# Kernel optimization log

Measured on AMD Instinct MI355X. Metric: run time of the kernel, lower is better.

Reference implementation:

```python
import jax, jax.numpy as jnp
import numpy as np

B, S, E, H = 4, 2048, 2048, 16
D = E // H  # head_dim = 128
MAX_LEN = 2048


def _make_freqs():
    # standard RoPE frequencies: theta = 10000^{-2i/D}
    inv_freq = 1.0 / (10000.0 ** (np.arange(0, D, 2, dtype=np.float32) / D))  # [D/2]
    t = np.arange(MAX_LEN, dtype=np.float32)
    ang = np.outer(t, inv_freq)  # [max_len, D/2]
    cos = ang.reshape(1, MAX_LEN, 1, D // 2)
    return jnp.asarray(np.cos(cos)), jnp.asarray(np.sin(cos))


def setup_inputs() -> dict:
    key = jax.random.key(0)
    ks = jax.random.split(key, 10)
    sc = 1.0 / np.sqrt(E)
    freqs_cos, freqs_sin = _make_freqs()
    return {
        "x": jax.random.normal(ks[0], (B, S, E), dtype=jnp.float32),
        "freqs_cos": freqs_cos,
        "freqs_sin": freqs_sin,
        "wq": jax.random.normal(ks[1], (E, E), dtype=jnp.float32) * sc,
        "bq": jax.random.normal(ks[2], (E,), dtype=jnp.float32) * 0.01,
        "wk": jax.random.normal(ks[3], (E, E), dtype=jnp.float32) * sc,
        "bk": jax.random.normal(ks[4], (E,), dtype=jnp.float32) * 0.01,
        "wv": jax.random.normal(ks[5], (E, E), dtype=jnp.float32) * sc,
        "bv": jax.random.normal(ks[6], (E,), dtype=jnp.float32) * 0.01,
        "wo": jax.random.normal(ks[7], (E, E), dtype=jnp.float32) * sc,
        "bo": jax.random.normal(ks[8], (E,), dtype=jnp.float32) * 0.01,
    }


def _rope(t, cos, sin):
    # t: [B, S, H, D]; complex multiply on interleaved (even, odd) pairs
    tr = t.reshape(*t.shape[:-1], -1, 2)  # [B,S,H,D/2,2]
    xr, xi = tr[..., 0], tr[..., 1]
    rr = xr * cos - xi * sin
    ri = xr * sin + xi * cos
    return jnp.stack([rr, ri], axis=-1).reshape(t.shape)


def reference(x, freqs_cos, freqs_sin, wq, bq, wk, bk, wv, bv, wo, bo):
    b, s, _ = x.shape
    q = (x @ wq.T + bq).reshape(b, s, H, D)
    k = (x @ wk.T + bk).reshape(b, s, H, D)
    v = (x @ wv.T + bv).reshape(b, s, H, D)
    cos, sin = freqs_cos[:, :s], freqs_sin[:, :s]
    q = _rope(q, cos, sin)
    k = _rope(k, cos, sin)
    # FAITHFUL to source: q,k,v stay [B,S,H,D], so matmul contracts over D
    # producing per-position head-head scores [B,S,H,H] (no transpose to BHSD).
    qk = jnp.einsum("bshd,bsgd->bshg", q, k) / jnp.sqrt(jnp.float32(D))
    att = jax.nn.softmax(qk, axis=-1)
    att_out = jnp.einsum("bshg,bsgd->bshd", att, v)  # [B,S,H,D]
    # torch: transpose(1,2).contiguous().view(B,S,-1) -> h-major flatten
    att_out = jnp.transpose(att_out, (0, 2, 1, 3)).reshape(b, s, -1)
    return att_out @ wo.T + bo
```

## Files before the change

kernel.cpp:

```cpp
#include <hip/hip_runtime.h>
#include <stdint.h>

typedef unsigned short u16t;
typedef __attribute__((ext_vector_type(8))) short frag8;
typedef __attribute__((ext_vector_type(4))) float facc4;

#define S_LEN 2048
#define E_DIM 2048

__device__ __forceinline__ u16t f2bf(float f) {
    union { float f; uint32_t u; } c; c.f = f;
    return (u16t)((c.u + 0x7fffu + ((c.u >> 16) & 1u)) >> 16);
}

__global__ __launch_bounds__(256) void cvt_kernel(const float* __restrict__ src,
                                                  u16t* __restrict__ dst, int n4) {
    int i = blockIdx.x * 256 + threadIdx.x;
    if (i >= n4) return;
    float4 v = ((const float4*)src)[i];
    ushort4 o;
    o.x = f2bf(v.x); o.y = f2bf(v.y); o.z = f2bf(v.z); o.w = f2bf(v.w);
    ((ushort4*)dst)[i] = o;
}

__device__ __forceinline__ void gldl16(const u16t* g, u16t* l) {
    __builtin_amdgcn_global_load_lds(
        (__attribute__((address_space(1))) void*)(g),
        (__attribute__((address_space(3))) void*)(l), 16, 0, 0);
}

__device__ __forceinline__ void gemm_core(const u16t* __restrict__ A,
                                          const u16t* __restrict__ Bw,
                                          u16t* As0, u16t* As1,
                                          u16t* Bs0, u16t* Bs1,
                                          facc4 acc[4][8]) {
    const int t    = threadIdx.x;
    const int lane = t & 63;
    const int wid  = t >> 6;
    const int m16  = lane & 15;
    const int quad = lane >> 4;
    const int sw   = (m16 >> 1) & 3;
    const int wm   = (wid & 1) * 64;
    const int wn   = (wid >> 1) * 128;
    const size_t bm0 = (size_t)blockIdx.y * 128;
    const size_t bn0 = (size_t)blockIdx.x * 256;

#pragma unroll
    for (int i = 0; i < 4; ++i)
#pragma unroll
        for (int j = 0; j < 8; ++j) acc[i][j] = facc4{0.f, 0.f, 0.f, 0.f};

    const u16t* Ab = A + bm0 * E_DIM;
    const u16t* Bb = Bw + bn0 * E_DIM;

    const int l8 = lane * 8;
    const int rA0 = ((wid * 1024 + l8) >> 5);
    const int rA1 = rA0 + 16;
    const int rB0 = ((wid * 2048 + l8) >> 5);
    const int rB1 = rB0 + 16, rB2 = rB0 + 32, rB3 = rB0 + 48;
    const int c3 = lane & 3;
    const size_t gA0 = (size_t)rA0 * E_DIM + ((c3 ^ ((rA0 >> 1) & 3)) * 8);
    const size_t gA1 = (size_t)rA1 * E_DIM + ((c3 ^ ((rA1 >> 1) & 3)) * 8);
    const size_t gB0 = (size_t)rB0 * E_DIM + ((c3 ^ ((rB0 >> 1) & 3)) * 8);
    const size_t gB1 = (size_t)rB1 * E_DIM + ((c3 ^ ((rB1 >> 1) & 3)) * 8);
    const size_t gB2 = (size_t)rB2 * E_DIM + ((c3 ^ ((rB2 >> 1) & 3)) * 8);
    const size_t gB3 = (size_t)rB3 * E_DIM + ((c3 ^ ((rB3 >> 1) & 3)) * 8);
    u16t* lA0 = As0 + wid * 1024;
    u16t* lA1 = As1 + wid * 1024;
    u16t* lB0 = Bs0 + wid * 2048;
    u16t* lB1 = Bs1 + wid * 2048;

    for (int k0 = 0; k0 < E_DIM; k0 += 64) {
        __syncthreads();
        gldl16(Ab + gA0 + k0,      lA0);
        gldl16(Ab + gA1 + k0,      lA0 + 512);
        gldl16(Ab + gA0 + k0 + 32, lA1);
        gldl16(Ab + gA1 + k0 + 32, lA1 + 512);
        gldl16(Bb + gB0 + k0,      lB0);
        gldl16(Bb + gB1 + k0,      lB0 + 512);
        gldl16(Bb + gB2 + k0,      lB0 + 1024);
        gldl16(Bb + gB3 + k0,      lB0 + 1536);
        gldl16(Bb + gB0 + k0 + 32, lB1);
        gldl16(Bb + gB1 + k0 + 32, lB1 + 512);
        gldl16(Bb + gB2 + k0 + 32, lB1 + 1024);
        gldl16(Bb + gB3 + k0 + 32, lB1 + 1536);
        __syncthreads();

#pragma unroll
        for (int h = 0; h < 2; ++h) {
            const u16t* Ah = h ? As1 : As0;
            const u16t* Bh = h ? Bs1 : Bs0;
            frag8 av[4], bv[8];
#pragma unroll
            for (int i = 0; i < 4; ++i)
                av[i] = *(const frag8*)(Ah + (wm + i * 16 + m16) * 32 + (quad ^ sw) * 8);
#pragma unroll
            for (int j = 0; j < 8; ++j)
                bv[j] = *(const frag8*)(Bh + (wn + j * 16 + m16) * 32 + (quad ^ sw) * 8);
#pragma unroll
            for (int i = 0; i < 4; ++i)
#pragma unroll
                for (int j = 0; j < 8; ++j)
                    acc[i][j] = __builtin_amdgcn_mfma_f32_16x16x32_bf16(
                        av[i], bv[j], acc[i][j], 0, 0, 0);
        }
    }
}

struct QkvArgs {
    const u16t* w[3];
    const float* bias[3];
    u16t* out[3];
};

__global__ __launch_bounds__(256, 2)
void qkv_gemm(const u16t* __restrict__ xb, QkvArgs args,
              const float* __restrict__ fcos, const float* __restrict__ fsin) {
    __shared__ u16t As0[128 * 32], As1[128 * 32];
    __shared__ u16t Bs0[256 * 32], Bs1[256 * 32];
    facc4 acc[4][8];
    const int z = blockIdx.z;
    gemm_core(xb, args.w[z], As0, As1, Bs0, Bs1, acc);

    const int t    = threadIdx.x;
    const int lane = t & 63;
    const int m16  = lane & 15;
    const int quad = lane >> 4;
    const int wid  = t >> 6;
    const int wm   = (wid & 1) * 64;
    const int wn   = (wid >> 1) * 128;
    const int bm0  = blockIdx.y * 128;
    const int bn0  = blockIdx.x * 256;
    const bool rope = (z < 2);
    u16t* out = args.out[z];
    const float* bias = args.bias[z];

#pragma unroll
    for (int i = 0; i < 4; ++i) {
#pragma unroll
        for (int j = 0; j < 8; ++j) {
            const int n = bn0 + wn + j * 16 + m16;
            const float bn_ = bias[n];
#pragma unroll
            for (int r = 0; r < 4; ++r) {
                const int m = bm0 + wm + i * 16 + quad * 4 + r;
                float v = acc[i][j][r] + bn_;
                const float part = __shfl_xor(v, 1, 64);
                if (rope) {
                    const int s = m & (S_LEN - 1);
                    const int p = (n & 127) >> 1;
                    const float cs = fcos[s * 64 + p];
                    const float sn = fsin[s * 64 + p];
                    v = (n & 1) ? (part * sn + v * cs) : (v * cs - part * sn);
                }
                out[(size_t)m * E_DIM + n] = f2bf(v);
            }
        }
    }
}

__global__ __launch_bounds__(256, 2)
void out_gemm(const u16t* __restrict__ sh, const u16t* __restrict__ wob,
              const float* __restrict__ bo, float* __restrict__ out) {
    __shared__ u16t As0[128 * 32], As1[128 * 32];
    __shared__ u16t Bs0[256 * 32], Bs1[256 * 32];
    facc4 acc[4][8];
    gemm_core(sh, wob, As0, As1, Bs0, Bs1, acc);

    const int t    = threadIdx.x;
    const int lane = t & 63;
    const int m16  = lane & 15;
    const int quad = lane >> 4;
    const int wid  = t >> 6;
    const int wm   = (wid & 1) * 64;
    const int wn   = (wid >> 1) * 128;
    const int bm0  = blockIdx.y * 128;
    const int bn0  = blockIdx.x * 256;

#pragma unroll
    for (int i = 0; i < 4; ++i) {
#pragma unroll
        for (int j = 0; j < 8; ++j) {
            const int n = bn0 + wn + j * 16 + m16;
            const float bn_ = bo[n];
#pragma unroll
            for (int r = 0; r < 4; ++r) {
                const int m = bm0 + wm + i * 16 + quad * 4 + r;
                out[(size_t)m * E_DIM + n] = acc[i][j][r] + bn_;
            }
        }
    }
}

__global__ __launch_bounds__(256)
void attn_kernel(const u16t* __restrict__ qb, const u16t* __restrict__ kb,
                 const u16t* __restrict__ vb, u16t* __restrict__ sh) {
    __shared__ u16t Vs[4][16 * 136];
    __shared__ u16t Pt[4][16 * 32];

    const int t    = threadIdx.x;
    const int wid  = t >> 6;
    const int lane = t & 63;
    const int m16  = lane & 15;
    const int quad = lane >> 4;
    const int tk   = blockIdx.x * 4 + wid;
    const int b    = tk >> 11;
    const int s    = tk & (S_LEN - 1);
    const size_t row = (size_t)tk * E_DIM;

    frag8 aq[4], ak[4];
    const u16t* qrow = qb + row + m16 * 128 + quad * 8;
    const u16t* krow = kb + row + m16 * 128 + quad * 8;
#pragma unroll
    for (int ks = 0; ks < 4; ++ks) {
        aq[ks] = *(const frag8*)(qrow + ks * 32);
        ak[ks] = *(const frag8*)(krow + ks * 32);
    }

    u16t* vs = Vs[wid];
#pragma unroll
    for (int c = 0; c < 4; ++c) {
        const int e  = c * 512 + lane * 8;
        const int vr = e >> 7, vc = e & 127;
        *(uint4*)(vs + vr * 136 + vc) = *(const uint4*)(vb + row + e);
    }

    facc4 sacc = facc4{0.f, 0.f, 0.f, 0.f};
#pragma unroll
    for (int ks = 0; ks < 4; ++ks)
        sacc = __builtin_amdgcn_mfma_f32_16x16x32_bf16(aq[ks], ak[ks], sacc, 0, 0, 0);

    float p[4], mx[4], sm[4];
#pragma unroll
    for (int r = 0; r < 4; ++r) { p[r] = sacc[r] * 0.08838834764831845f; mx[r] = p[r]; }
#pragma unroll
    for (int msk = 1; msk < 16; msk <<= 1)
#pragma unroll
        for (int r = 0; r < 4; ++r) mx[r] = fmaxf(mx[r], __shfl_xor(mx[r], msk, 64));
#pragma unroll
    for (int r = 0; r < 4; ++r) { p[r] = __expf(p[r] - mx[r]); sm[r] = p[r]; }
#pragma unroll
    for (int msk = 1; msk < 16; msk <<= 1)
#pragma unroll
        for (int r = 0; r < 4; ++r) sm[r] += __shfl_xor(sm[r], msk, 64);

    u16t* pt = Pt[wid];
#pragma unroll
    for (int r = 0; r < 4; ++r)
        pt[(quad * 4 + r) * 32 + m16] = f2bf(p[r] / sm[r]);
    *(uint2*)(pt + m16 * 32 + 16 + quad * 4) = uint2{0u, 0u};

    __syncthreads();

    const frag8 aP = *(const frag8*)(pt + m16 * 32 + quad * 8);

    facc4 oacc[8];
#pragma unroll
    for (int d = 0; d < 8; ++d) oacc[d] = facc4{0.f, 0.f, 0.f, 0.f};
#pragma unroll
    for (int dblk = 0; dblk < 8; ++dblk) {
        union { u16t u[8]; frag8 f; } bb;
#pragma unroll
        for (int j = 0; j < 8; ++j)
            bb.u[j] = vs[((quad * 8 + j) & 15) * 136 + dblk * 16 + m16];
        oacc[dblk] = __builtin_amdgcn_mfma_f32_16x16x32_bf16(aP, bb.f, oacc[dblk], 0, 0, 0);
    }

    const size_t base = ((size_t)b << 22) + (size_t)(s >> 4) * E_DIM
                      + (size_t)((s & 15) * 128);
#pragma unroll
    for (int dblk = 0; dblk < 8; ++dblk) {
        const int d = dblk * 16 + m16;
#pragma unroll
        for (int r = 0; r < 4; ++r) {
            const int h = quad * 4 + r;
            sh[base + ((size_t)h << 18) + d] = f2bf(oacc[dblk][r]);
        }
    }
}

extern "C" void kernel_launch(void* const* d_in, const int* in_sizes, int n_in,
                              void* d_out, int out_size, void* d_ws, size_t ws_size,
                              hipStream_t stream) {
    const float* x    = (const float*)d_in[0];
    const float* fcos = (const float*)d_in[1];
    const float* fsin = (const float*)d_in[2];
    const float* wq   = (const float*)d_in[3];
    const float* bq   = (const float*)d_in[4];
    const float* wk   = (const float*)d_in[5];
    const float* bk   = (const float*)d_in[6];
    const float* wv   = (const float*)d_in[7];
    const float* bv   = (const float*)d_in[8];
    const float* wo   = (const float*)d_in[9];
    const float* bo   = (const float*)d_in[10];
    float* out = (float*)d_out;

    char* ws = (char*)d_ws;
    u16t* xb  = (u16t*)(ws);
    u16t* qb  = (u16t*)(ws + 33554432ull);
    u16t* kb  = (u16t*)(ws + 67108864ull);
    u16t* vb  = (u16t*)(ws + 100663296ull);
    u16t* wqb = (u16t*)(ws + 134217728ull);
    u16t* wkb = (u16t*)(ws + 142606336ull);
    u16t* wvb = (u16t*)(ws + 150994944ull);
    u16t* wob = (u16t*)(ws + 159383552ull);

    cvt_kernel<<<16384, 256, 0, stream>>>(x, xb, 4194304);
    cvt_kernel<<<4096, 256, 0, stream>>>(wq, wqb, 1048576);
    cvt_kernel<<<4096, 256, 0, stream>>>(wk, wkb, 1048576);
    cvt_kernel<<<4096, 256, 0, stream>>>(wv, wvb, 1048576);
    cvt_kernel<<<4096, 256, 0, stream>>>(wo, wob, 1048576);

    QkvArgs qa;
    qa.w[0] = wqb; qa.w[1] = wkb; qa.w[2] = wvb;
    qa.bias[0] = bq; qa.bias[1] = bk; qa.bias[2] = bv;
    qa.out[0] = qb; qa.out[1] = kb; qa.out[2] = vb;
    qkv_gemm<<<dim3(8, 64, 3), 256, 0, stream>>>(xb, qa, fcos, fsin);

    attn_kernel<<<2048, 256, 0, stream>>>(qb, kb, vb, xb);

    out_gemm<<<dim3(8, 64), 256, 0, stream>>>(xb, wob, bo, out);
}
```

Measured before the change: 526.2 us.

## Shrink GEMM K-step, coalesce attention stores, merge weight conversions

The shared GEMM core now stages a 32-wide K slice per iteration instead of 64, which halves LDS use but doubles the number of block barriers and load rounds. The attention kernel replaces a block-wide barrier with a wave barrier around its per-wave probability tile. It also stages its output through LDS so each lane writes 16-byte rows, where before it made scattered 2-byte stores. The four weight bf16 conversions are folded into one launch indexed by blockIdx.y. The smaller K slice may reduce latency hiding in the GEMMs, and reusing the V tile for output staging relies on it being private to each wave.

```diff
diff --git a/kernel.cpp b/kernel.cpp
--- a/kernel.cpp
+++ b/kernel.cpp
@@ -23,6 +23,17 @@
     ((ushort4*)dst)[i] = o;
 }
 
+struct CvtPtrs { const float* s[4]; u16t* d[4]; };
+__global__ __launch_bounds__(256) void cvt4_kernel(CvtPtrs p, int n4) {
+    int i = blockIdx.x * 256 + threadIdx.x;
+    if (i >= n4) return;
+    const int w = blockIdx.y;
+    float4 v = ((const float4*)p.s[w])[i];
+    ushort4 o;
+    o.x = f2bf(v.x); o.y = f2bf(v.y); o.z = f2bf(v.z); o.w = f2bf(v.w);
+    ((ushort4*)p.d[w])[i] = o;
+}
+
 __device__ __forceinline__ void gldl16(const u16t* g, u16t* l) {
     __builtin_amdgcn_global_load_lds(
         (__attribute__((address_space(1))) void*)(g),
@@ -31,8 +42,7 @@
 
 __device__ __forceinline__ void gemm_core(const u16t* __restrict__ A,
                                           const u16t* __restrict__ Bw,
-                                          u16t* As0, u16t* As1,
-                                          u16t* Bs0, u16t* Bs1,
+                                          u16t* As, u16t* Bs,
                                           facc4 acc[4][8]) {
     const int t    = threadIdx.x;
     const int lane = t & 63;
@@ -54,9 +64,9 @@
     const u16t* Bb = Bw + bn0 * E_DIM;
 
     const int l8 = lane * 8;
-    const int rA0 = ((wid * 1024 + l8) >> 5);
+    const int rA0 = (wid * 1024 + l8) >> 5;
     const int rA1 = rA0 + 16;
-    const int rB0 = ((wid * 2048 + l8) >> 5);
+    const int rB0 = (wid * 2048 + l8) >> 5;
     const int rB1 = rB0 + 16, rB2 = rB0 + 32, rB3 = rB0 + 48;
     const int c3 = lane & 3;
     const size_t gA0 = (size_t)rA0 * E_DIM + ((c3 ^ ((rA0 >> 1) & 3)) * 8);
@@ -65,45 +75,32 @@
     const size_t gB1 = (size_t)rB1 * E_DIM + ((c3 ^ ((rB1 >> 1) & 3)) * 8);
     const size_t gB2 = (size_t)rB2 * E_DIM + ((c3 ^ ((rB2 >> 1) & 3)) * 8);
     const size_t gB3 = (size_t)rB3 * E_DIM + ((c3 ^ ((rB3 >> 1) & 3)) * 8);
-    u16t* lA0 = As0 + wid * 1024;
-    u16t* lA1 = As1 + wid * 1024;
-    u16t* lB0 = Bs0 + wid * 2048;
-    u16t* lB1 = Bs1 + wid * 2048;
-
-    for (int k0 = 0; k0 < E_DIM; k0 += 64) {
+    u16t* lA = As + wid * 1024;
+    u16t* lB = Bs + wid * 2048;
+
+    for (int k0 = 0; k0 < E_DIM; k0 += 32) {
         __syncthreads();
-        gldl16(Ab + gA0 + k0,      lA0);
-        gldl16(Ab + gA1 + k0,      lA0 + 512);
-        gldl16(Ab + gA0 + k0 + 32, lA1);
-        gldl16(Ab + gA1 + k0 + 32, lA1 + 512);
-        gldl16(Bb + gB0 + k0,      lB0);
-        gldl16(Bb + gB1 + k0,      lB0 + 512);
-        gldl16(Bb + gB2 + k0,      lB0 + 1024);
-        gldl16(Bb + gB3 + k0,      lB0 + 1536);
-        gldl16(Bb + gB0 + k0 + 32, lB1);
-        gldl16(Bb + gB1 + k0 + 32, lB1 + 512);
-        gldl16(Bb + gB2 + k0 + 32, lB1 + 1024);
-        gldl16(Bb + gB3 + k0 + 32, lB1 + 1536);
+        gldl16(Ab + gA0 + k0, lA);
+        gldl16(Ab + gA1 + k0, lA + 512);
+        gldl16(Bb + gB0 + k0, lB);
+        gldl16(Bb + gB1 + k0, lB + 512);
+        gldl16(Bb + gB2 + k0, lB + 1024);
+        gldl16(Bb + gB3 + k0, lB + 1536);
         __syncthreads();
 
-#pragma unroll
-        for (int h = 0; h < 2; ++h) {
-            const u16t* Ah = h ? As1 : As0;
-            const u16t* Bh = h ? Bs1 : Bs0;
-            frag8 av[4], bv[8];
-#pragma unroll
-            for (int i = 0; i < 4; ++i)
-                av[i] = *(const frag8*)(Ah + (wm + i * 16 + m16) * 32 + (quad ^ sw) * 8);
+        frag8 av[4], bv[8];
+#pragma unroll
+        for (int i = 0; i < 4; ++i)
+            av[i] = *(const frag8*)(As + (wm + i * 16 + m16) * 32 + (quad ^ sw) * 8);
+#pragma unroll
+        for (int j = 0; j < 8; ++j)
+            bv[j] = *(const frag8*)(Bs + (wn + j * 16 + m16) * 32 + (quad ^ sw) * 8);
+#pragma unroll
+        for (int i = 0; i < 4; ++i)
 #pragma unroll
             for (int j = 0; j < 8; ++j)
-                bv[j] = *(const frag8*)(Bh + (wn + j * 16 + m16) * 32 + (quad ^ sw) * 8);
-#pragma unroll
-            for (int i = 0; i < 4; ++i)
-#pragma unroll
-                for (int j = 0; j < 8; ++j)
-                    acc[i][j] = __builtin_amdgcn_mfma_f32_16x16x32_bf16(
-                        av[i], bv[j], acc[i][j], 0, 0, 0);
-        }
+                acc[i][j] = __builtin_amdgcn_mfma_f32_16x16x32_bf16(
+                    av[i], bv[j], acc[i][j], 0, 0, 0);
     }
 }
 
@@ -116,11 +113,11 @@
 __global__ __launch_bounds__(256, 2)
 void qkv_gemm(const u16t* __restrict__ xb, QkvArgs args,
               const float* __restrict__ fcos, const float* __restrict__ fsin) {
-    __shared__ u16t As0[128 * 32], As1[128 * 32];
-    __shared__ u16t Bs0[256 * 32], Bs1[256 * 32];
+    __shared__ u16t As[128 * 32];
+    __shared__ u16t Bs[256 * 32];
     facc4 acc[4][8];
     const int z = blockIdx.z;
-    gemm_core(xb, args.w[z], As0, As1, Bs0, Bs1, acc);
+    gemm_core(xb, args.w[z], As, Bs, acc);
 
     const int t    = threadIdx.x;
     const int lane = t & 63;
@@ -162,10 +159,10 @@
 __global__ __launch_bounds__(256, 2)
 void out_gemm(const u16t* __restrict__ sh, const u16t* __restrict__ wob,
               const float* __restrict__ bo, float* __restrict__ out) {
-    __shared__ u16t As0[128 * 32], As1[128 * 32];
-    __shared__ u16t Bs0[256 * 32], Bs1[256 * 32];
+    __shared__ u16t As[128 * 32];
+    __shared__ u16t Bs[256 * 32];
     facc4 acc[4][8];
-    gemm_core(sh, wob, As0, As1, Bs0, Bs1, acc);
+    gemm_core(sh, wob, As, Bs, acc);
 
     const int t    = threadIdx.x;
     const int lane = t & 63;
@@ -250,7 +247,7 @@
         pt[(quad * 4 + r) * 32 + m16] = f2bf(p[r] / sm[r]);
     *(uint2*)(pt + m16 * 32 + 16 + quad * 4) = uint2{0u, 0u};
 
-    __syncthreads();
+    __builtin_amdgcn_wave_barrier();
 
     const frag8 aP = *(const frag8*)(pt + m16 * 32 + quad * 8);
 
@@ -266,16 +263,21 @@
         oacc[dblk] = __builtin_amdgcn_mfma_f32_16x16x32_bf16(aP, bb.f, oacc[dblk], 0, 0, 0);
     }
 
+    __builtin_amdgcn_wave_barrier();
+#pragma unroll
+    for (int dblk = 0; dblk < 8; ++dblk)
+#pragma unroll
+        for (int r = 0; r < 4; ++r)
+            vs[(quad * 4 + r) * 136 + dblk * 16 + m16] = f2bf(oacc[dblk][r]);
+    __builtin_amdgcn_wave_barrier();
+
     const size_t base = ((size_t)b << 22) + (size_t)(s >> 4) * E_DIM
                       + (size_t)((s & 15) * 128);
 #pragma unroll
-    for (int dblk = 0; dblk < 8; ++dblk) {
-        const int d = dblk * 16 + m16;
-#pragma unroll
-        for (int r = 0; r < 4; ++r) {
-            const int h = quad * 4 + r;
-            sh[base + ((size_t)h << 18) + d] = f2bf(oacc[dblk][r]);
-        }
+    for (int hb = 0; hb < 4; ++hb) {
+        const int h = hb * 4 + quad;
+        const uint4 ov = *(const uint4*)(vs + h * 136 + m16 * 8);
+        *(uint4*)(sh + base + ((size_t)h << 18) + m16 * 8) = ov;
     }
 }
 
@@ -306,10 +308,10 @@
     u16t* wob = (u16t*)(ws + 159383552ull);
 
     cvt_kernel<<<16384, 256, 0, stream>>>(x, xb, 4194304);
-    cvt_kernel<<<4096, 256, 0, stream>>>(wq, wqb, 1048576);
-    cvt_kernel<<<4096, 256, 0, stream>>>(wk, wkb, 1048576);
-    cvt_kernel<<<4096, 256, 0, stream>>>(wv, wvb, 1048576);
-    cvt_kernel<<<4096, 256, 0, stream>>>(wo, wob, 1048576);
+    CvtPtrs cp;
+    cp.s[0] = wq; cp.s[1] = wk; cp.s[2] = wv; cp.s[3] = wo;
+    cp.d[0] = wqb; cp.d[1] = wkb; cp.d[2] = wvb; cp.d[3] = wob;
+    cvt4_kernel<<<dim3(4096, 4), 256, 0, stream>>>(cp, 1048576);
 
     QkvArgs qa;
     qa.w[0] = wqb; qa.w[1] = wkb; qa.w[2] = wvb;
```

Measured after the change: 539.9 us. 1.03x slower.
